# Optimization experiments

Hardware: AMD Instinct MI355X
Metric: run time of the kernel (lower is better)

Reference implementation:

```python
import jax, jax.numpy as jnp
import numpy as np
from jax import lax

EPS = 1e-5

def conv2d(x, w, b=None, pad=1):
    # x: [N,C,H,W], w: [O,I,kh,kw]
    out = lax.conv_general_dilated(x, w, window_strides=(1, 1),
                                   padding=[(pad, pad), (pad, pad)],
                                   dimension_numbers=('NCHW', 'OIHW', 'NCHW'))
    if b is not None:
        out = out + b[None, :, None, None]
    return out

def batchnorm(x, gamma, beta):
    # training-mode BN (biased batch stats), matching torch default train()
    mean = jnp.mean(x, axis=(0, 2, 3), keepdims=True)
    var = jnp.var(x, axis=(0, 2, 3), keepdims=True)
    xn = (x - mean) * lax.rsqrt(var + EPS)
    return xn * gamma[None, :, None, None] + beta[None, :, None, None]

def setup_inputs() -> dict:
    key = jax.random.key(0)
    ks = jax.random.split(key, 16)
    B, Cin, H, W = 4, 3, 256, 256
    Cout = 128
    NP = 32
    npat = NP // 3  # 10 per normal region
    qc_in = Cout + 3 * npat + NP  # 190 (actual concat width)

    def kaiming(k, shape, fan_in):
        return jax.random.normal(k, shape, jnp.float32) * np.sqrt(2.0 / fan_in)

    inp = {
        'x': jax.random.normal(ks[0], (B, Cin, H, W), jnp.float32),
        'conv1_w': kaiming(ks[1], (Cout // 2, Cin, 3, 3), Cin * 9),
        'conv1_b': jnp.zeros((Cout // 2,), jnp.float32),
        'bn1_g': jnp.ones((Cout // 2,), jnp.float32),
        'bn1_b': jnp.zeros((Cout // 2,), jnp.float32),
        'conv2_w': kaiming(ks[2], (Cout, Cout // 2, 3, 3), (Cout // 2) * 9),
        'conv2_b': jnp.zeros((Cout,), jnp.float32),
        'bn2_g': jnp.ones((Cout,), jnp.float32),
        'bn2_b': jnp.zeros((Cout,), jnp.float32),
        'core_p': jax.random.normal(ks[3], (npat, Cout, 3, 3), jnp.float32),
        'clad_p': jax.random.normal(ks[4], (npat, Cout, 3, 3), jnp.float32),
        'ferr_p': jax.random.normal(ks[5], (npat, Cout, 3, 3), jnp.float32),
        'anom_p': jax.random.normal(ks[6], (NP, Cout, 3, 3), jnp.float32),
        'qa1_w': kaiming(ks[7], (64, qc_in, 1, 1), qc_in),
        'qa1_b': jnp.zeros((64,), jnp.float32),
        'qa2_w': kaiming(ks[8], (1, 64, 1, 1), 64),
        'qa2_b': jnp.zeros((1,), jnp.float32),
        'cls_w': kaiming(ks[9], (4, qc_in, 1, 1), qc_in),
        'cls_b': jnp.zeros((4,), jnp.float32),
    }
    return inp

def reference(x, conv1_w, conv1_b, bn1_g, bn1_b, conv2_w, conv2_b, bn2_g, bn2_b,
              core_p, clad_p, ferr_p, anom_p, qa1_w, qa1_b, qa2_w, qa2_b, cls_w, cls_b):
    # feature extractor: conv-bn-relu x2
    h = jax.nn.relu(batchnorm(conv2d(x, conv1_w, conv1_b), bn1_g, bn1_b))
    features = jax.nn.relu(batchnorm(conv2d(h, conv2_w, conv2_b), bn2_g, bn2_b))

    # pattern matching: the per-pattern loop of 1-out-channel convs + sigmoid
    # is exactly one multi-output-channel conv (no bias) + sigmoid
    normal_w = jnp.concatenate([core_p, clad_p, ferr_p], axis=0)  # [30,C,3,3]
    all_matches = jax.nn.sigmoid(conv2d(features, normal_w))       # [B,30,H,W]
    anomaly_matches = jax.nn.sigmoid(conv2d(features, anom_p))     # [B,32,H,W]

    quality_input = jnp.concatenate([features, all_matches, anomaly_matches], axis=1)
    q = jax.nn.relu(conv2d(quality_input, qa1_w, qa1_b, pad=0))
    quality_scores = jax.nn.sigmoid(conv2d(q, qa2_w, qa2_b, pad=0))

    classifications = conv2d(quality_input, cls_w, cls_b, pad=0)
    region_logits = classifications[:, :3]
    anomaly_logits = classifications[:, 3:4]
    region_probs = jax.nn.softmax(region_logits, axis=1)
    anomaly_probs = jax.nn.sigmoid(anomaly_logits)

    return (features, region_logits, anomaly_logits, all_matches,
            anomaly_matches, quality_scores, region_probs, anomaly_probs)
```

## Files before the change

### kernel.cpp

```cpp
#include <hip/hip_runtime.h>
#include <hip/hip_bf16.h>

typedef unsigned short u16;
typedef __attribute__((ext_vector_type(8)))  short s8v;
typedef __attribute__((ext_vector_type(4)))  short s4v;
typedef __attribute__((ext_vector_type(16))) float f16v;

#define HWX 65536
#define EPSV 1e-5f

#define O0 0u
#define O1 33554432u
#define O2 34340864u
#define O3 34603008u
#define O4 42467328u
#define O5 50855936u
#define O6 51118080u
#define O7 51904512u

__device__ __forceinline__ float u2f(u16 u) {
    union { unsigned int i; float f; } v; v.i = ((unsigned int)u) << 16; return v.f;
}
__device__ __forceinline__ u16 f2u(float f) {
    __hip_bfloat16 h = __float2bfloat16(f);
    return *reinterpret_cast<u16*>(&h);
}
__device__ __forceinline__ s8v ld8(const u16* p) {
    union { s8v v; s4v h[2]; } r;
    r.h[0] = *(const s4v*)p;
    r.h[1] = *(const s4v*)(p + 4);
    return r.v;
}

#define PHYS(i) ((i) + ((i) >> 5))

__global__ __launch_bounds__(256) void k_conv1(const float* __restrict__ x,
                                               const float* __restrict__ w,
                                               const float* __restrict__ bias,
                                               u16* __restrict__ out,
                                               float* __restrict__ ssum,
                                               float* __restrict__ sqsum) {
    const int h = blockIdx.x, cb = blockIdx.y, b = blockIdx.z;
    const int t = threadIdx.x;
    const int pg = t & 31, cg = t >> 5;
    const int px0 = pg * 8, c0 = cg * 4;
    const int cbase = cb * 32;

    __shared__ float xs[3][3][266];
    __shared__ float wl[27 * 33];

    float acc[4][8];
    #pragma unroll
    for (int c = 0; c < 4; c++) {
        float bv = bias[cbase + c0 + c];
        #pragma unroll
        for (int p = 0; p < 8; p++) acc[c][p] = bv;
    }

    for (int idx = t; idx < 3 * 768; idx += 256) {
        int ci = idx / 768, rem = idx - ci * 768;
        int r = rem >> 8, px = rem & 255;
        int hh = h + r - 1;
        float v = 0.f;
        if ((unsigned)hh < 256u)
            v = x[((size_t)(b * 3 + ci) * 256 + hh) * 256 + px];
        xs[ci][r][PHYS(1 + px)] = v;
    }
    if (t < 18) {
        int ci = t / 6, rr = t - ci * 6;
        xs[ci][rr >> 1][(rr & 1) ? PHYS(257) : 0] = 0.f;
    }
    for (int idx = t; idx < 27 * 32; idx += 256) {
        int co = idx / 27, rem = idx - co * 27;
        wl[rem * 33 + co] = w[(cbase + co) * 27 + rem];
    }
    __syncthreads();

    for (int ci = 0; ci < 3; ci++) {
        #pragma unroll
        for (int kh = 0; kh < 3; kh++) {
            float xv[10];
            #pragma unroll
            for (int j = 0; j < 10; j++) xv[j] = xs[ci][kh][PHYS(px0 + j)];
            float wv[3][4];
            #pragma unroll
            for (int kw = 0; kw < 3; kw++)
                #pragma unroll
                for (int c = 0; c < 4; c++)
                    wv[kw][c] = wl[(ci * 9 + kh * 3 + kw) * 33 + c0 + c];
            #pragma unroll
            for (int c = 0; c < 4; c++)
                #pragma unroll
                for (int p = 0; p < 8; p++)
                    acc[c][p] += xv[p] * wv[0][c] + xv[p + 1] * wv[1][c]
                               + xv[p + 2] * wv[2][c];
        }
    }

    #pragma unroll
    for (int c = 0; c < 4; c++) {
        int cm = cbase + c0 + c;
        u16* op = out + (((size_t)(b * 64 + cm) * 256 + h) * 256 + px0);
        #pragma unroll
        for (int p = 0; p < 8; p++) op[p] = f2u(acc[c][p]);
    }

    __syncthreads();
    float* red = &xs[0][0][0];
    #pragma unroll
    for (int c = 0; c < 4; c++) {
        float sv = 0.f, qv = 0.f;
        #pragma unroll
        for (int p = 0; p < 8; p++) { sv += acc[c][p]; qv += acc[c][p] * acc[c][p]; }
        red[(c0 + c) * 33 + pg] = sv;
        red[1056 + (c0 + c) * 33 + pg] = qv;
    }
    __syncthreads();
    if (t < 64) {
        int co = t & 31, v = t >> 5;
        const float* base = red + v * 1056 + co * 33;
        float sum = 0.f;
        #pragma unroll
        for (int i = 0; i < 32; i++) sum += base[i];
        atomicAdd((v ? sqsum : ssum) + cbase + co, sum);
    }
}

__global__ void k_finalize(const float* __restrict__ s, const float* __restrict__ q,
                           const float* __restrict__ g, const float* __restrict__ be,
                           float* __restrict__ sc, float* __restrict__ sh, int C) {
    int c = threadIdx.x;
    if (c >= C) return;
    const float invN = 1.f / 262144.f;
    float m = s[c] * invN;
    float v = fmaxf(q[c] * invN - m * m, 0.f);
    float scale = g[c] * rsqrtf(v + EPSV);
    sc[c] = scale;
    sh[c] = be[c] - m * scale;
}

__global__ __launch_bounds__(256) void k_bnrelu_h(ushort4* __restrict__ buf,
                                                  const float* __restrict__ sc,
                                                  const float* __restrict__ sh) {
    size_t i = (size_t)blockIdx.x * 256 + threadIdx.x;
    int c = (int)(i >> 14) & 63;
    float s = sc[c], h0 = sh[c];
    ushort4 r = buf[i];
    ushort4 o;
    o.x = f2u(fmaxf(u2f(r.x) * s + h0, 0.f));
    o.y = f2u(fmaxf(u2f(r.y) * s + h0, 0.f));
    o.z = f2u(fmaxf(u2f(r.z) * s + h0, 0.f));
    o.w = f2u(fmaxf(u2f(r.w) * s + h0, 0.f));
    buf[i] = o;
}

__global__ __launch_bounds__(256) void k_bnrelu(float4* __restrict__ buf,
                                                const float* __restrict__ sc,
                                                const float* __restrict__ sh, int C) {
    size_t i = (size_t)blockIdx.x * 256 + threadIdx.x;
    int c = (int)(i >> 14) % C;
    float s = sc[c], h0 = sh[c];
    float4 r = buf[i];
    float4 o;
    o.x = fmaxf(r.x * s + h0, 0.f);
    o.y = fmaxf(r.y * s + h0, 0.f);
    o.z = fmaxf(r.z * s + h0, 0.f);
    o.w = fmaxf(r.w * s + h0, 0.f);
    buf[i] = o;
}

__global__ __launch_bounds__(256) void k_stats(const float* __restrict__ raw,
                                               float* __restrict__ ssum,
                                               float* __restrict__ sqsum) {
    const int co = blockIdx.x, seg = blockIdx.y;
    const int t = threadIdx.x;
    __shared__ float red[8];
    float s = 0.f, q = 0.f;
    for (int b = 0; b < 4; b++) {
        const float4* p = (const float4*)(raw + ((size_t)(b * 128 + co) * HWX) + seg * 8192);
        for (int i = t; i < 2048; i += 256) {
            float4 v = p[i];
            s += v.x + v.y + v.z + v.w;
            q += v.x * v.x + v.y * v.y + v.z * v.z + v.w * v.w;
        }
    }
    #pragma unroll
    for (int off = 32; off; off >>= 1) {
        s += __shfl_down(s, off, 64);
        q += __shfl_down(q, off, 64);
    }
    int lane = t & 63, wv = t >> 6;
    if (lane == 0) { red[wv] = s; red[4 + wv] = q; }
    __syncthreads();
    if (t == 0) atomicAdd(&ssum[co], red[0] + red[1] + red[2] + red[3]);
    else if (t == 1) atomicAdd(&sqsum[co], red[4] + red[5] + red[6] + red[7]);
}

__global__ void k_prep_w(const float* __restrict__ wcat, u16* __restrict__ wtile) {
    int i = blockIdx.x * 256 + threadIdx.x;
    if (i >= 159744) return;
    int ch = i / 19968, rem = i - ch * 19968;
    int pl = rem / 9984; rem -= pl * 9984;
    int kwco = rem / 52, k = rem - kwco * 52;
    int kw = kwco >> 6, co = kwco & 63;
    u16 v = 0;
    if (k < 48 && co < 62) {
        int kh = k >> 4, ci = ch * 16 + (k & 15);
        float f = wcat[(size_t)co * 1152 + ci * 9 + kh * 3 + kw];
        u16 hv = f2u(f);
        v = pl ? f2u(f - u2f(hv)) : hv;
    }
    wtile[i] = v;
}
__global__ void k_prep_w2(const float* __restrict__ w2, u16* __restrict__ wtile2) {
    int i = blockIdx.x * 256 + threadIdx.x;
    if (i >= 79872) return;
    int ch = i / 19968, rem = i - ch * 19968;
    int kwco = rem / 52, k = rem - kwco * 52;
    int kw = kwco >> 7, co = kwco & 127;
    u16 v = 0;
    if (k < 48) {
        int kh = k >> 4, ci = ch * 16 + (k & 15);
        v = f2u(w2[((size_t)co * 64 + ci) * 9 + kh * 3 + kw]);
    }
    wtile2[i] = v;
}
__global__ void k_prep_wh(const float* __restrict__ qa1w, const float* __restrict__ clsw,
                          u16* __restrict__ whl) {
    int i = blockIdx.x * 256 + threadIdx.x;
    if (i >= 46080) return;
    int ch = i / 3840, rem = i - ch * 3840;
    int pl = rem / 1920; rem -= pl * 1920;
    int co = rem / 20, kloc = rem - co * 20;
    u16 v = 0;
    int k = ch * 16 + kloc;
    if (kloc < 16 && k < 190 && co < 68) {
        float f = (co < 64) ? qa1w[co * 190 + k] : clsw[(co - 64) * 190 + k];
        u16 hv = f2u(f);
        v = pl ? f2u(f - u2f(hv)) : hv;
    }
    whl[i] = v;
}

__device__ __forceinline__ void load_x_c2(const u16* __restrict__ hb, int b, int ch,
                                          int h, int t, unsigned xp[24]) {
    #pragma unroll
    for (int r = 0; r < 3; r++) {
        int hh = h + r - 1;
        bool vr = (unsigned)hh < 256u;
        if (vr) {
            const u16* base = hb + ((size_t)(b * 64 + ch * 16) << 16)
                            + ((size_t)hh << 8) + t;
            #pragma unroll
            for (int ci = 0; ci < 16; ci += 2) {
                unsigned a = base[(size_t)ci << 16];
                unsigned c = base[(size_t)(ci + 1) << 16];
                xp[(r * 16 + ci) >> 1] = a | (c << 16);
            }
        } else {
            #pragma unroll
            for (int ci = 0; ci < 16; ci += 2) xp[(r * 16 + ci) >> 1] = 0u;
        }
    }
}

__device__ __forceinline__ void load_x_match(const float* __restrict__ feat, int b, int ch,
                                             int h, int t, float xv[48]) {
    #pragma unroll
    for (int r = 0; r < 3; r++) {
        int hh = h + r - 1;
        bool vr = (unsigned)hh < 256u;
        if (vr) {
            const float* base = feat + ((size_t)(b * 128 + ch * 16) << 16)
                              + ((size_t)hh << 8) + t;
            #pragma unroll
            for (int ci = 0; ci < 16; ci++)
                xv[r * 16 + ci] = base[(size_t)ci << 16];
        } else {
            #pragma unroll
            for (int ci = 0; ci < 16; ci++) xv[r * 16 + ci] = 0.f;
        }
    }
}

__global__ __launch_bounds__(256, 2) void k_conv2_mf(
    const u16* __restrict__ hb, const u16* __restrict__ wtile2,
    const float* __restrict__ bias, float* __restrict__ out)
{
    const int h = blockIdx.x, b = blockIdx.y;
    const int t = threadIdx.x, l = t & 63, wv = t >> 6;
    const int kg = (l >> 5) * 8, nn = l & 31;

    __shared__ __align__(16) u16 xs[258 * 52];
    __shared__ __align__(16) u16 wl[3 * 128 * 52];

    f16v acc[2][4];
    #pragma unroll
    for (int pt = 0; pt < 2; pt++)
        #pragma unroll
        for (int s = 0; s < 4; s++)
            #pragma unroll
            for (int r = 0; r < 16; r++) acc[pt][s][r] = 0.f;

    for (int i = t; i < 258 * 52 / 4; i += 256)
        ((ushort4*)xs)[i] = ushort4{0, 0, 0, 0};
    __syncthreads();

    unsigned xp[24];
    load_x_c2(hb, b, 0, h, t, xp);

    for (int ch = 0; ch < 4; ch++) {
        {
            const int4* src = (const int4*)(wtile2 + (size_t)ch * 19968);
            for (int i = t; i < 2496; i += 256) ((int4*)wl)[i] = src[i];
        }
        #pragma unroll
        for (int r = 0; r < 3; r++) {
            if ((unsigned)(h + r - 1) < 256u) {
                #pragma unroll
                for (int g = 0; g < 4; g++) {
                    int i0 = r * 16 + g * 4;
                    uint2 hp;
                    hp.x = xp[i0 >> 1];
                    hp.y = xp[(i0 >> 1) + 1];
                    *(uint2*)&xs[(size_t)(t + 1) * 52 + i0] = hp;
                }
            }
        }
        __syncthreads();
        if (ch < 3) load_x_c2(hb, b, ch + 1, h, t, xp);
        #pragma unroll
        for (int kw = 0; kw < 3; kw++) {
            #pragma unroll
            for (int ks = 0; ks < 3; ks++) {
                int k0 = ks * 16 + kg;
                s8v af[4], bf[2];
                #pragma unroll
                for (int s = 0; s < 4; s++)
                    af[s] = ld8(&wl[(kw * 128 + s * 32 + nn) * 52 + k0]);
                #pragma unroll
                for (int pt = 0; pt < 2; pt++)
                    bf[pt] = ld8(&xs[((wv * 2 + pt) * 32 + nn + kw) * 52 + k0]);
                #pragma unroll
                for (int pt = 0; pt < 2; pt++)
                    #pragma unroll
                    for (int s = 0; s < 4; s++)
                        acc[pt][s] = __builtin_amdgcn_mfma_f32_32x32x16_bf16(
                            af[s], bf[pt], acc[pt][s], 0, 0, 0);
            }
        }
        __syncthreads();
    }

    #pragma unroll
    for (int pt = 0; pt < 2; pt++) {
        int px = (wv * 2 + pt) * 32 + nn;
        #pragma unroll
        for (int s = 0; s < 4; s++) {
            #pragma unroll
            for (int r = 0; r < 16; r++) {
                int co = s * 32 + (r & 3) + 8 * (r >> 2) + 4 * (l >> 5);
                out[(((size_t)b * 128 + co) * 256 + h) * 256 + px] = acc[pt][s][r] + bias[co];
            }
        }
    }
}

__global__ __launch_bounds__(256, 2) void k_match_mf(
    const float* __restrict__ feat, const u16* __restrict__ wtile,
    float* __restrict__ out_all, float* __restrict__ out_anom)
{
    const int h = blockIdx.x, b = blockIdx.y;
    const int t = threadIdx.x, l = t & 63, wv = t >> 6;
    const int kg = (l >> 5) * 8, nn = l & 31;

    __shared__ __align__(16) u16 xs[258 * 52];
    __shared__ __align__(16) u16 wl[2][9984];

    f16v acc[2][2];
    #pragma unroll
    for (int pt = 0; pt < 2; pt++)
        #pragma unroll
        for (int s = 0; s < 2; s++)
            #pragma unroll
            for (int r = 0; r < 16; r++) acc[pt][s][r] = 0.f;

    for (int i = t; i < 258 * 52 / 4; i += 256)
        ((ushort4*)xs)[i] = ushort4{0, 0, 0, 0};
    __syncthreads();

    float xv[48];
    load_x_match(feat, b, 0, h, t, xv);
    unsigned lor[24];

    for (int ch = 0; ch < 8; ch++) {
        {
            const int4* src = (const int4*)(wtile + (size_t)ch * 2 * 9984);
            for (int i = t; i < 2496; i += 256) ((int4*)wl[0])[i] = src[i];
        }
        #pragma unroll
        for (int r = 0; r < 3; r++) {
            bool vr = (unsigned)(h + r - 1) < 256u;
            #pragma unroll
            for (int g = 0; g < 4; g++) {
                int i0 = r * 16 + g * 4;
                u16 h0 = f2u(xv[i0 + 0]), h1 = f2u(xv[i0 + 1]);
                u16 h2 = f2u(xv[i0 + 2]), h3 = f2u(xv[i0 + 3]);
                lor[(i0 >> 1) + 0] = (unsigned)f2u(xv[i0 + 0] - u2f(h0))
                                   | ((unsigned)f2u(xv[i0 + 1] - u2f(h1)) << 16);
                lor[(i0 >> 1) + 1] = (unsigned)f2u(xv[i0 + 2] - u2f(h2))
                                   | ((unsigned)f2u(xv[i0 + 3] - u2f(h3)) << 16);
                if (vr) {
                    uint2 hp;
                    hp.x = (unsigned)h0 | ((unsigned)h1 << 16);
                    hp.y = (unsigned)h2 | ((unsigned)h3 << 16);
                    *(uint2*)&xs[(size_t)(t + 1) * 52 + i0] = hp;
                }
            }
        }
        __syncthreads();
        if (ch < 7) load_x_match(feat, b, ch + 1, h, t, xv);
        #pragma unroll
        for (int kw = 0; kw < 3; kw++) {
            #pragma unroll
            for (int ks = 0; ks < 3; ks++) {
                int k0 = ks * 16 + kg;
                s8v xfr[2];
                #pragma unroll
                for (int pt = 0; pt < 2; pt++)
                    xfr[pt] = ld8(&xs[((wv * 2 + pt) * 32 + nn + kw) * 52 + k0]);
                s8v ah0 = ld8(&wl[0][(kw * 64 + nn) * 52 + k0]);
                s8v ah1 = ld8(&wl[0][(kw * 64 + 32 + nn) * 52 + k0]);
                s8v al0 = ld8(&wl[1][(kw * 64 + nn) * 52 + k0]);
                s8v al1 = ld8(&wl[1][(kw * 64 + 32 + nn) * 52 + k0]);
                #pragma unroll
                for (int pt = 0; pt < 2; pt++) {
                    acc[pt][0] = __builtin_amdgcn_mfma_f32_32x32x16_bf16(ah0, xfr[pt], acc[pt][0], 0, 0, 0);
                    acc[pt][0] = __builtin_amdgcn_mfma_f32_32x32x16_bf16(al0, xfr[pt], acc[pt][0], 0, 0, 0);
                    acc[pt][1] = __builtin_amdgcn_mfma_f32_32x32x16_bf16(ah1, xfr[pt], acc[pt][1], 0, 0, 0);
                    acc[pt][1] = __builtin_amdgcn_mfma_f32_32x32x16_bf16(al1, xfr[pt], acc[pt][1], 0, 0, 0);
                }
            }
        }
        __syncthreads();
        #pragma unroll
        for (int r = 0; r < 3; r++) {
            if ((unsigned)(h + r - 1) < 256u) {
                #pragma unroll
                for (int g = 0; g < 4; g++) {
                    int i0 = r * 16 + g * 4;
                    uint2 lp;
                    lp.x = lor[i0 >> 1];
                    lp.y = lor[(i0 >> 1) + 1];
                    *(uint2*)&xs[(size_t)(t + 1) * 52 + i0] = lp;
                }
            }
        }
        __syncthreads();
        #pragma unroll
        for (int kw = 0; kw < 3; kw++) {
            #pragma unroll
            for (int ks = 0; ks < 3; ks++) {
                int k0 = ks * 16 + kg;
                s8v xfr[2];
                #pragma unroll
                for (int pt = 0; pt < 2; pt++)
                    xfr[pt] = ld8(&xs[((wv * 2 + pt) * 32 + nn + kw) * 52 + k0]);
                s8v ah0 = ld8(&wl[0][(kw * 64 + nn) * 52 + k0]);
                s8v ah1 = ld8(&wl[0][(kw * 64 + 32 + nn) * 52 + k0]);
                #pragma unroll
                for (int pt = 0; pt < 2; pt++) {
                    acc[pt][0] = __builtin_amdgcn_mfma_f32_32x32x16_bf16(ah0, xfr[pt], acc[pt][0], 0, 0, 0);
                    acc[pt][1] = __builtin_amdgcn_mfma_f32_32x32x16_bf16(ah1, xfr[pt], acc[pt][1], 0, 0, 0);
                }
            }
        }
        __syncthreads();
    }

    #pragma unroll
    for (int pt = 0; pt < 2; pt++) {
        int px = (wv * 2 + pt) * 32 + nn;
        #pragma unroll
        for (int s = 0; s < 2; s++) {
            #pragma unroll
            for (int r = 0; r < 16; r++) {
                int cm = s * 32 + (r & 3) + 8 * (r >> 2) + 4 * (l >> 5);
                float sg = 1.f / (1.f + __expf(-acc[pt][s][r]));
                if (cm < 30)
                    out_all[(((size_t)b * 30 + cm) * 256 + h) * 256 + px] = sg;
                else if (cm < 62)
                    out_anom[(((size_t)b * 32 + cm - 30) * 256 + h) * 256 + px] = sg;
            }
        }
    }
}

__device__ __forceinline__ void load_x_heads(const float* __restrict__ fb,
                                             const float* __restrict__ ab,
                                             const float* __restrict__ nb,
                                             int ch, float xv[16]) {
    #pragma unroll
    for (int ci = 0; ci < 16; ci++) {
        int k = ch * 16 + ci;
        float v;
        if (k < 128)      v = fb[(size_t)k << 16];
        else if (k < 158) v = ab[(size_t)(k - 128) << 16];
        else if (k < 190) v = nb[(size_t)(k - 158) << 16];
        else              v = 0.f;
        xv[ci] = v;
    }
}

__global__ __launch_bounds__(256, 2) void k_heads_mf(
    const float* __restrict__ dout, const u16* __restrict__ whl,
    const float* __restrict__ qa1b, const float* __restrict__ qa2w,
    const float* __restrict__ qa2b, const float* __restrict__ clsb,
    float* __restrict__ out)
{
    const int h = blockIdx.x, b = blockIdx.y;
    const int t = threadIdx.x, l = t & 63, wv = t >> 6;
    const int kg = (l >> 5) * 8, nn = l & 31;

    __shared__ __align__(16) u16 xh[256 * 20];
    __shared__ __align__(16) u16 xl[256 * 20];
    __shared__ __align__(16) u16 wl2[2 * 1920];
    __shared__ float lb[69];
    __shared__ float lw2[64];

    if (t < 64) { lb[t] = qa1b[t]; lw2[t] = qa2w[t]; }
    if (t < 4) lb[64 + t] = clsb[t];
    if (t == 0) lb[68] = qa2b[0];

    f16v acc[3][2];
    #pragma unroll
    for (int s = 0; s < 3; s++)
        #pragma unroll
        for (int pt = 0; pt < 2; pt++)
            #pragma unroll
            for (int r = 0; r < 16; r++) acc[s][pt][r] = 0.f;

    const float* fb = dout + O0 + (((size_t)b * 128) << 16) + ((size_t)h << 8) + t;
    const float* ab = dout + O3 + (((size_t)b * 30) << 16) + ((size_t)h << 8) + t;
    const float* nb = dout + O4 + (((size_t)b * 32) << 16) + ((size_t)h << 8) + t;

    float xv[16];
    load_x_heads(fb, ab, nb, 0, xv);

    #pragma unroll
    for (int ch = 0; ch < 12; ch++) {
        {
            const int4* src = (const int4*)(whl + (size_t)ch * 3840);
            for (int i = t; i < 480; i += 256) ((int4*)wl2)[i] = src[i];
        }
        #pragma unroll
        for (int g = 0; g < 4; g++) {
            int i0 = g * 4;
            u16 h0 = f2u(xv[i0 + 0]), h1 = f2u(xv[i0 + 1]);
            u16 h2 = f2u(xv[i0 + 2]), h3 = f2u(xv[i0 + 3]);
            uint2 hp, lp;
            hp.x = (unsigned)h0 | ((unsigned)h1 << 16);
            hp.y = (unsigned)h2 | ((unsigned)h3 << 16);
            lp.x = (unsigned)f2u(xv[i0 + 0] - u2f(h0))
                 | ((unsigned)f2u(xv[i0 + 1] - u2f(h1)) << 16);
            lp.y = (unsigned)f2u(xv[i0 + 2] - u2f(h2))
                 | ((unsigned)f2u(xv[i0 + 3] - u2f(h3)) << 16);
            *(uint2*)&xh[t * 20 + i0] = hp;
            *(uint2*)&xl[t * 20 + i0] = lp;
        }
        __syncthreads();
        if (ch < 11) load_x_heads(fb, ab, nb, ch + 1, xv);
        s8v xfh[2], xfl[2];
        #pragma unroll
        for (int pt = 0; pt < 2; pt++) {
            int row = (wv * 2 + pt) * 32 + nn;
            xfh[pt] = ld8(&xh[row * 20 + kg]);
            xfl[pt] = ld8(&xl[row * 20 + kg]);
        }
        #pragma unroll
        for (int s = 0; s < 3; s++) {
            s8v awh = ld8(&wl2[(s * 32 + nn) * 20 + kg]);
            s8v awl = ld8(&wl2[1920 + (s * 32 + nn) * 20 + kg]);
            #pragma unroll
            for (int pt = 0; pt < 2; pt++) {
                acc[s][pt] = __builtin_amdgcn_mfma_f32_32x32x16_bf16(awh, xfh[pt], acc[s][pt], 0, 0, 0);
                acc[s][pt] = __builtin_amdgcn_mfma_f32_32x32x16_bf16(awl, xfh[pt], acc[s][pt], 0, 0, 0);
                acc[s][pt] = __builtin_amdgcn_mfma_f32_32x32x16_bf16(awh, xfl[pt], acc[s][pt], 0, 0, 0);
            }
        }
        __syncthreads();
    }

    const int hi = l >> 5;
    #pragma unroll
    for (int pt = 0; pt < 2; pt++) {
        float qa_part = 0.f;
        #pragma unroll
        for (int m = 0; m < 2; m++)
            #pragma unroll
            for (int r = 0; r < 16; r++) {
                int row = m * 32 + (r & 3) + 8 * (r >> 2) + 4 * hi;
                float v = acc[m][pt][r] + lb[row];
                qa_part += fmaxf(v, 0.f) * lw2[row];
            }
        qa_part += __shfl_xor(qa_part, 32, 64);
        if (hi == 0) {
            int px = (wv * 2 + pt) * 32 + nn;
            size_t hw = (size_t)h * 256 + px;
            float quality = 1.f / (1.f + __expf(-(qa_part + lb[68])));
            float c0 = acc[2][pt][0] + lb[64];
            float c1 = acc[2][pt][1] + lb[65];
            float c2 = acc[2][pt][2] + lb[66];
            float c3 = acc[2][pt][3] + lb[67];
            float m0 = fmaxf(c0, fmaxf(c1, c2));
            float e0 = __expf(c0 - m0), e1 = __expf(c1 - m0), e2 = __expf(c2 - m0);
            float inv = 1.f / (e0 + e1 + e2);
            out[O1 + ((size_t)b * 3 + 0) * HWX + hw] = c0;
            out[O1 + ((size_t)b * 3 + 1) * HWX + hw] = c1;
            out[O1 + ((size_t)b * 3 + 2) * HWX + hw] = c2;
            out[O2 + (size_t)b * HWX + hw] = c3;
            out[O5 + (size_t)b * HWX + hw] = quality;
            out[O6 + ((size_t)b * 3 + 0) * HWX + hw] = e0 * inv;
            out[O6 + ((size_t)b * 3 + 1) * HWX + hw] = e1 * inv;
            out[O6 + ((size_t)b * 3 + 2) * HWX + hw] = e2 * inv;
            out[O7 + (size_t)b * HWX + hw] = 1.f / (1.f + __expf(-c3));
        }
    }
}

extern "C" void kernel_launch(void* const* d_in, const int* in_sizes, int n_in,
                              void* d_out, int out_size, void* d_ws, size_t ws_size,
                              hipStream_t stream) {
    (void)in_sizes; (void)n_in; (void)out_size; (void)ws_size;
    const float* x    = (const float*)d_in[0];
    const float* w1   = (const float*)d_in[1];
    const float* b1   = (const float*)d_in[2];
    const float* g1   = (const float*)d_in[3];
    const float* be1  = (const float*)d_in[4];
    const float* w2   = (const float*)d_in[5];
    const float* b2   = (const float*)d_in[6];
    const float* g2   = (const float*)d_in[7];
    const float* be2  = (const float*)d_in[8];
    const float* core = (const float*)d_in[9];
    const float* clad = (const float*)d_in[10];
    const float* ferr = (const float*)d_in[11];
    const float* anom = (const float*)d_in[12];
    const float* qa1w = (const float*)d_in[13];
    const float* qa1b = (const float*)d_in[14];
    const float* qa2w = (const float*)d_in[15];
    const float* qa2b = (const float*)d_in[16];
    const float* clsw = (const float*)d_in[17];
    const float* clsb = (const float*)d_in[18];

    char* ws = (char*)d_ws;
    float* stats = (float*)ws;
    float* s1 = stats + 0;
    float* q1 = stats + 64;
    float* s2 = stats + 128;
    float* q2 = stats + 256;
    float* sc1 = stats + 384;
    float* sh1 = stats + 448;
    float* sc2 = stats + 512;
    float* sh2 = stats + 640;
    u16*   hraw   = (u16*)(ws + 4096);
    float* wcat   = (float*)(ws + 33558528ull);
    u16*   wtile2 = (u16*)(ws + 33844224ull);
    u16*   wtile  = (u16*)(ws + 34004224ull);
    u16*   whl    = (u16*)wcat;
    float* dout = (float*)d_out;

    hipMemsetAsync(stats, 0, 384 * sizeof(float), stream);
    hipMemcpyAsync(wcat,             core, 10 * 1152 * 4, hipMemcpyDeviceToDevice, stream);
    hipMemcpyAsync(wcat + 10 * 1152, clad, 10 * 1152 * 4, hipMemcpyDeviceToDevice, stream);
    hipMemcpyAsync(wcat + 20 * 1152, ferr, 10 * 1152 * 4, hipMemcpyDeviceToDevice, stream);
    hipMemcpyAsync(wcat + 30 * 1152, anom, 32 * 1152 * 4, hipMemcpyDeviceToDevice, stream);

    dim3 blk(256);
    k_prep_w2<<<312, blk, 0, stream>>>(w2, wtile2);
    k_prep_w<<<624, blk, 0, stream>>>(wcat, wtile);
    k_prep_wh<<<180, blk, 0, stream>>>(qa1w, clsw, whl);

    k_conv1<<<dim3(256, 2, 4), blk, 0, stream>>>(x, w1, b1, hraw, s1, q1);
    k_finalize<<<1, 128, 0, stream>>>(s1, q1, g1, be1, sc1, sh1, 64);
    k_bnrelu_h<<<16384, blk, 0, stream>>>((ushort4*)hraw, sc1, sh1);

    k_conv2_mf<<<dim3(256, 4), blk, 0, stream>>>(hraw, wtile2, b2, dout + O0);
    k_stats<<<dim3(128, 8), blk, 0, stream>>>(dout + O0, s2, q2);
    k_finalize<<<1, 128, 0, stream>>>(s2, q2, g2, be2, sc2, sh2, 128);
    k_bnrelu<<<32768, blk, 0, stream>>>((float4*)(dout + O0), sc2, sh2, 128);

    k_match_mf<<<dim3(256, 4), blk, 0, stream>>>(dout + O0, wtile, dout + O3, dout + O4);
    k_heads_mf<<<dim3(256, 4), blk, 0, stream>>>(dout, whl, qa1b, qa2w, qa2b, clsb, dout);
}
```

Measured before the change: 648.5 us.

## Compute two output rows per block in match conv to reuse input rows and weights

The pattern-matching conv now has each block produce two adjacent output rows. It loads a 4-row input halo instead of 3, stores it in a per-row LDS layout, and reuses each weight fragment across both rows. This halves the grid and cuts redundant global feature loads and weight tile copies per output row. The low-residual bf16 split is now recomputed from the fp32 registers instead of being held in a separate array. The next-chunk prefetch has moved to after the second barrier. In exchange there are more accumulator registers (doubled acc) and 64 fp32 staging registers, which may hurt occupancy, and the prefetch now overlaps only the low-part MFMA pass.

```diff
diff --git a/kernel.cpp b/kernel.cpp
--- a/kernel.cpp
+++ b/kernel.cpp
@@ -264,21 +264,17 @@
     }
 }
 
-__device__ __forceinline__ void load_x_match(const float* __restrict__ feat, int b, int ch,
-                                             int h, int t, float xv[48]) {
-    #pragma unroll
-    for (int r = 0; r < 3; r++) {
-        int hh = h + r - 1;
-        bool vr = (unsigned)hh < 256u;
-        if (vr) {
+__device__ __forceinline__ void load_x_match2(const float* __restrict__ feat, int b, int ch,
+                                              int h0, int t, float xw[64]) {
+    #pragma unroll
+    for (int r = 0; r < 4; r++) {
+        int hh = h0 + r - 1;
+        if ((unsigned)hh < 256u) {
             const float* base = feat + ((size_t)(b * 128 + ch * 16) << 16)
                               + ((size_t)hh << 8) + t;
             #pragma unroll
             for (int ci = 0; ci < 16; ci++)
-                xv[r * 16 + ci] = base[(size_t)ci << 16];
-        } else {
-            #pragma unroll
-            for (int ci = 0; ci < 16; ci++) xv[r * 16 + ci] = 0.f;
+                xw[r * 16 + ci] = base[(size_t)ci << 16];
         }
     }
 }
@@ -370,108 +366,112 @@
     const float* __restrict__ feat, const u16* __restrict__ wtile,
     float* __restrict__ out_all, float* __restrict__ out_anom)
 {
-    const int h = blockIdx.x, b = blockIdx.y;
+    const int h0 = blockIdx.x * 2, b = blockIdx.y;
     const int t = threadIdx.x, l = t & 63, wv = t >> 6;
     const int kg = (l >> 5) * 8, nn = l & 31;
 
-    __shared__ __align__(16) u16 xs[258 * 52];
-    __shared__ __align__(16) u16 wl[2][9984];
-
-    f16v acc[2][2];
-    #pragma unroll
-    for (int pt = 0; pt < 2; pt++)
-        #pragma unroll
-        for (int s = 0; s < 2; s++)
-            #pragma unroll
-            for (int r = 0; r < 16; r++) acc[pt][s][r] = 0.f;
-
-    for (int i = t; i < 258 * 52 / 4; i += 256)
-        ((ushort4*)xs)[i] = ushort4{0, 0, 0, 0};
+    __shared__ __align__(16) u16 xr[4 * 258 * 20];
+    __shared__ __align__(16) u16 wl[2 * 9984];
+
+    f16v acc[2][2][2];
+    #pragma unroll
+    for (int o = 0; o < 2; o++)
+        #pragma unroll
+        for (int pt = 0; pt < 2; pt++)
+            #pragma unroll
+            for (int s = 0; s < 2; s++)
+                #pragma unroll
+                for (int r = 0; r < 16; r++) acc[o][pt][s][r] = 0.f;
+
+    for (int i = t; i < 4 * 258 * 20 / 4; i += 256)
+        ((ushort4*)xr)[i] = ushort4{0, 0, 0, 0};
     __syncthreads();
 
-    float xv[48];
-    load_x_match(feat, b, 0, h, t, xv);
-    unsigned lor[24];
+    float xw[64];
+    load_x_match2(feat, b, 0, h0, t, xw);
 
     for (int ch = 0; ch < 8; ch++) {
         {
             const int4* src = (const int4*)(wtile + (size_t)ch * 2 * 9984);
-            for (int i = t; i < 2496; i += 256) ((int4*)wl[0])[i] = src[i];
-        }
-        #pragma unroll
-        for (int r = 0; r < 3; r++) {
-            bool vr = (unsigned)(h + r - 1) < 256u;
-            #pragma unroll
-            for (int g = 0; g < 4; g++) {
-                int i0 = r * 16 + g * 4;
-                u16 h0 = f2u(xv[i0 + 0]), h1 = f2u(xv[i0 + 1]);
-                u16 h2 = f2u(xv[i0 + 2]), h3 = f2u(xv[i0 + 3]);
-                lor[(i0 >> 1) + 0] = (unsigned)f2u(xv[i0 + 0] - u2f(h0))
-                                   | ((unsigned)f2u(xv[i0 + 1] - u2f(h1)) << 16);
-                lor[(i0 >> 1) + 1] = (unsigned)f2u(xv[i0 + 2] - u2f(h2))
-                                   | ((unsigned)f2u(xv[i0 + 3] - u2f(h3)) << 16);
-                if (vr) {
+            for (int i = t; i < 2496; i += 256) ((int4*)wl)[i] = src[i];
+        }
+        #pragma unroll
+        for (int r = 0; r < 4; r++) {
+            if ((unsigned)(h0 + r - 1) < 256u) {
+                u16* dst = xr + r * 5160 + (t + 1) * 20;
+                #pragma unroll
+                for (int g = 0; g < 4; g++) {
+                    int i0 = r * 16 + g * 4;
+                    u16 v0 = f2u(xw[i0 + 0]), v1 = f2u(xw[i0 + 1]);
+                    u16 v2 = f2u(xw[i0 + 2]), v3 = f2u(xw[i0 + 3]);
                     uint2 hp;
-                    hp.x = (unsigned)h0 | ((unsigned)h1 << 16);
-                    hp.y = (unsigned)h2 | ((unsigned)h3 << 16);
-                    *(uint2*)&xs[(size_t)(t + 1) * 52 + i0] = hp;
+                    hp.x = (unsigned)v0 | ((unsigned)v1 << 16);
+                    hp.y = (unsigned)v2 | ((unsigned)v3 << 16);
+                    *(uint2*)&dst[g * 4] = hp;
                 }
             }
         }
         __syncthreads();
-        if (ch < 7) load_x_match(feat, b, ch + 1, h, t, xv);
         #pragma unroll
         for (int kw = 0; kw < 3; kw++) {
             #pragma unroll
             for (int ks = 0; ks < 3; ks++) {
                 int k0 = ks * 16 + kg;
-                s8v xfr[2];
-                #pragma unroll
-                for (int pt = 0; pt < 2; pt++)
-                    xfr[pt] = ld8(&xs[((wv * 2 + pt) * 32 + nn + kw) * 52 + k0]);
-                s8v ah0 = ld8(&wl[0][(kw * 64 + nn) * 52 + k0]);
-                s8v ah1 = ld8(&wl[0][(kw * 64 + 32 + nn) * 52 + k0]);
-                s8v al0 = ld8(&wl[1][(kw * 64 + nn) * 52 + k0]);
-                s8v al1 = ld8(&wl[1][(kw * 64 + 32 + nn) * 52 + k0]);
-                #pragma unroll
-                for (int pt = 0; pt < 2; pt++) {
-                    acc[pt][0] = __builtin_amdgcn_mfma_f32_32x32x16_bf16(ah0, xfr[pt], acc[pt][0], 0, 0, 0);
-                    acc[pt][0] = __builtin_amdgcn_mfma_f32_32x32x16_bf16(al0, xfr[pt], acc[pt][0], 0, 0, 0);
-                    acc[pt][1] = __builtin_amdgcn_mfma_f32_32x32x16_bf16(ah1, xfr[pt], acc[pt][1], 0, 0, 0);
-                    acc[pt][1] = __builtin_amdgcn_mfma_f32_32x32x16_bf16(al1, xfr[pt], acc[pt][1], 0, 0, 0);
+                s8v ah0 = ld8(&wl[(kw * 64 + nn) * 52 + k0]);
+                s8v ah1 = ld8(&wl[(kw * 64 + 32 + nn) * 52 + k0]);
+                s8v al0 = ld8(&wl[9984 + (kw * 64 + nn) * 52 + k0]);
+                s8v al1 = ld8(&wl[9984 + (kw * 64 + 32 + nn) * 52 + k0]);
+                #pragma unroll
+                for (int o = 0; o < 2; o++) {
+                    #pragma unroll
+                    for (int pt = 0; pt < 2; pt++) {
+                        s8v xf = ld8(&xr[(ks + o) * 5160
+                                         + ((wv * 2 + pt) * 32 + nn + kw) * 20 + kg]);
+                        acc[o][pt][0] = __builtin_amdgcn_mfma_f32_32x32x16_bf16(ah0, xf, acc[o][pt][0], 0, 0, 0);
+                        acc[o][pt][0] = __builtin_amdgcn_mfma_f32_32x32x16_bf16(al0, xf, acc[o][pt][0], 0, 0, 0);
+                        acc[o][pt][1] = __builtin_amdgcn_mfma_f32_32x32x16_bf16(ah1, xf, acc[o][pt][1], 0, 0, 0);
+                        acc[o][pt][1] = __builtin_amdgcn_mfma_f32_32x32x16_bf16(al1, xf, acc[o][pt][1], 0, 0, 0);
+                    }
                 }
             }
         }
         __syncthreads();
         #pragma unroll
-        for (int r = 0; r < 3; r++) {
-            if ((unsigned)(h + r - 1) < 256u) {
+        for (int r = 0; r < 4; r++) {
+            if ((unsigned)(h0 + r - 1) < 256u) {
+                u16* dst = xr + r * 5160 + (t + 1) * 20;
                 #pragma unroll
                 for (int g = 0; g < 4; g++) {
                     int i0 = r * 16 + g * 4;
+                    u16 h0v = f2u(xw[i0 + 0]), h1v = f2u(xw[i0 + 1]);
+                    u16 h2v = f2u(xw[i0 + 2]), h3v = f2u(xw[i0 + 3]);
                     uint2 lp;
-                    lp.x = lor[i0 >> 1];
-                    lp.y = lor[(i0 >> 1) + 1];
-                    *(uint2*)&xs[(size_t)(t + 1) * 52 + i0] = lp;
+                    lp.x = (unsigned)f2u(xw[i0 + 0] - u2f(h0v))
+                         | ((unsigned)f2u(xw[i0 + 1] - u2f(h1v)) << 16);
+                    lp.y = (unsigned)f2u(xw[i0 + 2] - u2f(h2v))
+                         | ((unsigned)f2u(xw[i0 + 3] - u2f(h3v)) << 16);
+                    *(uint2*)&dst[g * 4] = lp;
                 }
             }
         }
         __syncthreads();
+        if (ch < 7) load_x_match2(feat, b, ch + 1, h0, t, xw);
         #pragma unroll
         for (int kw = 0; kw < 3; kw++) {
             #pragma unroll
             for (int ks = 0; ks < 3; ks++) {
                 int k0 = ks * 16 + kg;
-                s8v xfr[2];
-                #pragma unroll
-                for (int pt = 0; pt < 2; pt++)
-                    xfr[pt] = ld8(&xs[((wv * 2 + pt) * 32 + nn + kw) * 52 + k0]);
-                s8v ah0 = ld8(&wl[0][(kw * 64 + nn) * 52 + k0]);
-                s8v ah1 = ld8(&wl[0][(kw * 64 + 32 + nn) * 52 + k0]);
-                #pragma unroll
-                for (int pt = 0; pt < 2; pt++) {
-                    acc[pt][0] = __builtin_amdgcn_mfma_f32_32x32x16_bf16(ah0, xfr[pt], acc[pt][0], 0, 0, 0);
-                    acc[pt][1] = __builtin_amdgcn_mfma_f32_32x32x16_bf16(ah1, xfr[pt], acc[pt][1], 0, 0, 0);
+                s8v ah0 = ld8(&wl[(kw * 64 + nn) * 52 + k0]);
+                s8v ah1 = ld8(&wl[(kw * 64 + 32 + nn) * 52 + k0]);
+                #pragma unroll
+                for (int o = 0; o < 2; o++) {
+                    #pragma unroll
+                    for (int pt = 0; pt < 2; pt++) {
+                        s8v xf = ld8(&xr[(ks + o) * 5160
+                                         + ((wv * 2 + pt) * 32 + nn + kw) * 20 + kg]);
+                        acc[o][pt][0] = __builtin_amdgcn_mfma_f32_32x32x16_bf16(ah0, xf, acc[o][pt][0], 0, 0, 0);
+                        acc[o][pt][1] = __builtin_amdgcn_mfma_f32_32x32x16_bf16(ah1, xf, acc[o][pt][1], 0, 0, 0);
+                    }
                 }
             }
         }
@@ -479,18 +479,22 @@
     }
 
     #pragma unroll
-    for (int pt = 0; pt < 2; pt++) {
-        int px = (wv * 2 + pt) * 32 + nn;
-        #pragma unroll
-        for (int s = 0; s < 2; s++) {
-            #pragma unroll
-            for (int r = 0; r < 16; r++) {
-                int cm = s * 32 + (r & 3) + 8 * (r >> 2) + 4 * (l >> 5);
-                float sg = 1.f / (1.f + __expf(-acc[pt][s][r]));
-                if (cm < 30)
-                    out_all[(((size_t)b * 30 + cm) * 256 + h) * 256 + px] = sg;
-                else if (cm < 62)
-                    out_anom[(((size_t)b * 32 + cm - 30) * 256 + h) * 256 + px] = sg;
+    for (int o = 0; o < 2; o++) {
+        int h = h0 + o;
+        #pragma unroll
+        for (int pt = 0; pt < 2; pt++) {
+            int px = (wv * 2 + pt) * 32 + nn;
+            #pragma unroll
+            for (int s = 0; s < 2; s++) {
+                #pragma unroll
+                for (int r = 0; r < 16; r++) {
+                    int cm = s * 32 + (r & 3) + 8 * (r >> 2) + 4 * (l >> 5);
+                    float sg = 1.f / (1.f + __expf(-acc[o][pt][s][r]));
+                    if (cm < 30)
+                        out_all[(((size_t)b * 30 + cm) * 256 + h) * 256 + px] = sg;
+                    else if (cm < 62)
+                        out_anom[(((size_t)b * 32 + cm - 30) * 256 + h) * 256 + px] = sg;
+                }
             }
         }
     }
@@ -689,6 +693,6 @@
     k_finalize<<<1, 128, 0, stream>>>(s2, q2, g2, be2, sc2, sh2, 128);
     k_bnrelu<<<32768, blk, 0, stream>>>((float4*)(dout + O0), sc2, sh2, 128);
 
-    k_match_mf<<<dim3(256, 4), blk, 0, stream>>>(dout + O0, wtile, dout + O3, dout + O4);
+    k_match_mf<<<dim3(128, 4), blk, 0, stream>>>(dout + O0, wtile, dout + O3, dout + O4);
     k_heads_mf<<<dim3(256, 4), blk, 0, stream>>>(dout, whl, qa1b, qa2w, qa2b, clsb, dout);
 }
```

Result: slower. 695.3 us (+7.2%).
